# Kernel optimization log

Measured on AMD Instinct MI355X. Metric: run time of the kernel, lower is better.

Reference implementation:

```python
import jax, jax.numpy as jnp
import numpy as np

N, IN_C, HEADS, OUT_C = 100000, 128, 4, 64
E = 1600000
NEG_SLOPE = 0.2
BN_EPS = 1e-5


def setup_inputs() -> dict:
    key = jax.random.key(0)
    ks = jax.random.split(key, 8)
    x = jax.random.normal(ks[0], (N, IN_C), dtype=jnp.float32)
    edge_index = jax.random.randint(ks[1], (2, E), 0, N, dtype=jnp.int64)
    glorot = 1.0 / np.sqrt(IN_C)
    W = jax.random.uniform(ks[2], (IN_C, HEADS * OUT_C), dtype=jnp.float32, minval=-glorot, maxval=glorot)
    att_src = jax.random.normal(ks[3], (HEADS, OUT_C), dtype=jnp.float32) * 0.1
    att_dst = jax.random.normal(ks[4], (HEADS, OUT_C), dtype=jnp.float32) * 0.1
    bias = jnp.zeros((HEADS * OUT_C,), dtype=jnp.float32)
    gamma = jnp.ones((HEADS * OUT_C,), dtype=jnp.float32)
    beta = jnp.zeros((HEADS * OUT_C,), dtype=jnp.float32)
    return {"x": x, "edge_index": edge_index, "W": W, "att_src": att_src,
            "att_dst": att_dst, "bias": bias, "gamma": gamma, "beta": beta}


def reference(x, edge_index, W, att_src, att_dst, bias, gamma, beta):
    n = x.shape[0]
    h_dim, c_dim = att_src.shape
    # add self loops
    loops = jnp.arange(n, dtype=edge_index.dtype)
    src = jnp.concatenate([edge_index[0], loops])  # [Et]
    dst = jnp.concatenate([edge_index[1], loops])  # [Et]
    # linear projection per head
    h = (x @ W).reshape(n, h_dim, c_dim)  # [N,H,C]
    a_src = jnp.einsum('nhc,hc->nh', h, att_src)  # [N,H]
    a_dst = jnp.einsum('nhc,hc->nh', h, att_dst)  # [N,H]
    # edge-wise attention logits + LeakyReLU
    e = jax.nn.leaky_relu(a_src[src] + a_dst[dst], NEG_SLOPE)  # [Et,H]
    # segment softmax over destination neighborhoods
    m = jax.ops.segment_max(e, dst, num_segments=n)  # [N,H]
    e = jnp.exp(e - m[dst])
    denom = jax.ops.segment_sum(e, dst, num_segments=n)  # [N,H]
    alpha = e / (denom[dst] + 1e-16)  # [Et,H]
    # weighted scatter-add aggregation
    out = jax.ops.segment_sum(h[src] * alpha[:, :, None], dst, num_segments=n)  # [N,H,C]
    out = out.reshape(n, h_dim * c_dim) + bias
    # BatchNorm (training-mode batch statistics) + ELU
    mean = out.mean(axis=0)
    var = out.var(axis=0)
    out = gamma * (out - mean) * jax.lax.rsqrt(var + BN_EPS) + beta
    return jax.nn.elu(out)
```

## Files before the change

kernel.cpp:

```cpp
#include <hip/hip_runtime.h>

#define IN_C 128
#define HEADS 4
#define OUT_C 64
#define OUT_F 256
#define NEG_SLOPE 0.2f
#define BN_EPS 1e-5f
#define NBUCK 64
#define BSTRIDE 48

typedef __attribute__((ext_vector_type(8))) short short8;
typedef __attribute__((ext_vector_type(4))) float floatx4;

__device__ __forceinline__ unsigned short f2bf(float f) {
    unsigned u = __float_as_uint(f);
    u += 0x7FFF + ((u >> 16) & 1);
    return (unsigned short)(u >> 16);
}
__device__ __forceinline__ float bf2f(unsigned short u) {
    return __uint_as_float(((unsigned)u) << 16);
}

__global__ void wtprep_kernel(const float* __restrict__ W, unsigned short* __restrict__ Wp)
{
    int idx = blockIdx.x * blockDim.x + threadIdx.x;
    int j  = idx & 7;
    int l  = (idx >> 3) & 63;
    int nt = (idx >> 9) & 3;
    int kt = (idx >> 11) & 3;
    int w  = idx >> 13;
    int k   = kt * 32 + (l >> 4) * 8 + j;
    int col = w * 64 + nt * 16 + (l & 15);
    Wp[idx] = f2bf(W[(size_t)k * OUT_F + col]);
}

__global__ __launch_bounds__(256) void gemm_build_kernel(
    const float* __restrict__ x, const unsigned short* __restrict__ Wp,
    const float* __restrict__ att_src, const float* __restrict__ att_dst,
    unsigned short* __restrict__ h, float* __restrict__ a_src, float* __restrict__ a_dst,
    const int* __restrict__ ei, int* __restrict__ deg, int* __restrict__ srcs,
    int nbg, int n, int E)
{
    if ((int)blockIdx.x >= nbg) {
        int e = ((int)blockIdx.x - nbg) * 256 + (int)threadIdx.x;
        if (e < E) {
            int s = ei[e];
            int d = ei[E + e];
            int pos = atomicAdd(&deg[d], 1);
            if (pos < BSTRIDE) srcs[d * BSTRIDE + pos] = s;
        }
        return;
    }

    __shared__ unsigned short As[16][144];
    __shared__ unsigned short Hs[16][268];

    const int t = threadIdx.x;
    const int w = t >> 6;
    const int l = t & 63;
    const int quad = l >> 4;
    const int c15 = l & 15;
    const int base = blockIdx.x * 16;

    {
        const float4* xs = (const float4*)(x + (size_t)base * IN_C);
#pragma unroll
        for (int i = 0; i < 2; ++i) {
            int idx = t + i * 256;
            float4 v = xs[idx];
            int fi = idx * 4;
            int row = fi >> 7, k = fi & 127;
            ushort4 b;
            b.x = f2bf(v.x); b.y = f2bf(v.y); b.z = f2bf(v.z); b.w = f2bf(v.w);
            *(ushort4*)&As[row][k] = b;
        }
    }

    short8 bfrag[4][4];
#pragma unroll
    for (int kt = 0; kt < 4; ++kt)
#pragma unroll
        for (int nt = 0; nt < 4; ++nt)
            bfrag[kt][nt] = *(const short8*)(Wp + (((w * 4 + kt) * 4 + nt) << 9) + l * 8);

    __syncthreads();

    floatx4 acc[4] = {};
#pragma unroll
    for (int kt = 0; kt < 4; ++kt) {
        int k0 = kt * 32 + quad * 8;
        short8 afrag = *(const short8*)&As[c15][k0];
#pragma unroll
        for (int nt = 0; nt < 4; ++nt)
            acc[nt] = __builtin_amdgcn_mfma_f32_16x16x32_bf16(afrag, bfrag[kt][nt], acc[nt], 0, 0, 0);
    }

    float asum[4] = {0.f, 0.f, 0.f, 0.f}, adsum[4] = {0.f, 0.f, 0.f, 0.f};
#pragma unroll
    for (int nt = 0; nt < 4; ++nt) {
        int col = w * 64 + nt * 16 + c15;
        float aw = att_src[col];
        float dw = att_dst[col];
#pragma unroll
        for (int r = 0; r < 4; ++r) {
            float v = acc[nt][r];
            Hs[quad * 4 + r][col] = f2bf(v);
            asum[r] = fmaf(v, aw, asum[r]);
            adsum[r] = fmaf(v, dw, adsum[r]);
        }
    }
#pragma unroll
    for (int r = 0; r < 4; ++r) {
        float vs = asum[r], vd = adsum[r];
#pragma unroll
        for (int m = 1; m < 16; m <<= 1) {
            vs += __shfl_xor(vs, m, 64);
            vd += __shfl_xor(vd, m, 64);
        }
        if (c15 == 0) {
            int node = base + quad * 4 + r;
            a_src[(size_t)node * HEADS + w] = vs;
            a_dst[(size_t)node * HEADS + w] = vd;
        }
    }

    __syncthreads();
#pragma unroll
    for (int i = 0; i < 2; ++i) {
        int chunk = t + i * 256;
        int si = chunk * 8;
        int row = si >> 8, c0 = si & 255;
        int4 v = *(const int4*)&Hs[row][c0];
        *(int4*)(h + (size_t)(base + row) * OUT_F + c0) = v;
    }
}

__global__ __launch_bounds__(256) void agg_kernel(
    const unsigned short* __restrict__ h, const float* __restrict__ a_src,
    const float* __restrict__ a_dst, const int* __restrict__ deg,
    const int* __restrict__ srcs, const float* __restrict__ bias,
    float* __restrict__ out, float* __restrict__ sbuck, int n)
{
    __shared__ float red[2][4][OUT_F];

    int wave_in_blk = threadIdx.x >> 6;
    int lane = threadIdx.x & 63;
    int dst = blockIdx.x * 4 + wave_in_blk;
    int myh = lane >> 4;
    bool valid = (dst < n);

    float4 o4 = {0.f, 0.f, 0.f, 0.f};

    if (valid) {
        float adh = a_dst[(size_t)dst * HEADS + myh];

        float es = a_src[(size_t)dst * HEADS + myh] + adh;
        es = (es > 0.f) ? es : NEG_SLOPE * es;
        float wgt = __expf(es);
        ushort4 hv = ((const ushort4*)(h + (size_t)dst * OUT_F))[lane];
        float4 acc;
        acc.x = bf2f(hv.x) * wgt; acc.y = bf2f(hv.y) * wgt;
        acc.z = bf2f(hv.z) * wgt; acc.w = bf2f(hv.w) * wgt;
        float wsum = wgt;

        const int start = dst * BSTRIDE;
        int cnt = deg[dst];
        cnt = (cnt > BSTRIDE) ? BSTRIDE : cnt;
        const int last = start + cnt - 1;
        for (int j = 0; j < cnt; j += 8) {
            int rem = cnt - j;
            int s[8];
#pragma unroll
            for (int u = 0; u < 8; ++u) {
                int idx = start + j + u;
                s[u] = srcs[(idx < last) ? idx : last];
            }
            float ew[8];
#pragma unroll
            for (int u = 0; u < 8; ++u) ew[u] = a_src[(size_t)s[u] * HEADS + myh];
            ushort4 hh[8];
#pragma unroll
            for (int u = 0; u < 8; ++u) hh[u] = ((const ushort4*)(h + (size_t)s[u] * OUT_F))[lane];
#pragma unroll
            for (int u = 0; u < 8; ++u) {
                float e = ew[u] + adh;
                e = (e > 0.f) ? e : NEG_SLOPE * e;
                float wv = __expf(e);
                wv = (u < rem) ? wv : 0.f;
                acc.x = fmaf(bf2f(hh[u].x), wv, acc.x);
                acc.y = fmaf(bf2f(hh[u].y), wv, acc.y);
                acc.z = fmaf(bf2f(hh[u].z), wv, acc.z);
                acc.w = fmaf(bf2f(hh[u].w), wv, acc.w);
                wsum += wv;
            }
        }

        float inv = 1.f / (wsum + 1e-16f);
        float4 b4 = ((const float4*)bias)[lane];
        o4.x = fmaf(acc.x, inv, b4.x);
        o4.y = fmaf(acc.y, inv, b4.y);
        o4.z = fmaf(acc.z, inv, b4.z);
        o4.w = fmaf(acc.w, inv, b4.w);
        ((float4*)(out + (size_t)dst * OUT_F))[lane] = o4;
    }

    int c0 = lane * 4;
    *(float4*)&red[0][wave_in_blk][c0] = o4;
    float4 q4;
    q4.x = o4.x * o4.x; q4.y = o4.y * o4.y; q4.z = o4.z * o4.z; q4.w = o4.w * o4.w;
    *(float4*)&red[1][wave_in_blk][c0] = q4;
    __syncthreads();

    int t = threadIdx.x;
    float s  = red[0][0][t] + red[0][1][t] + red[0][2][t] + red[0][3][t];
    float s2 = red[1][0][t] + red[1][1][t] + red[1][2][t] + red[1][3][t];
    float* bk = sbuck + (size_t)(blockIdx.x & (NBUCK - 1)) * (2 * OUT_F);
    atomicAdd(&bk[t], s);
    atomicAdd(&bk[OUT_F + t], s2);
}

__global__ void statsfinal_kernel(const float* __restrict__ sbuck,
                                  const float* __restrict__ gamma,
                                  const float* __restrict__ beta,
                                  float* __restrict__ ss, int n)
{
    int c = threadIdx.x;
    float s = 0.f, s2 = 0.f;
    for (int b = 0; b < NBUCK; ++b) {
        s  += sbuck[(size_t)b * (2 * OUT_F) + c];
        s2 += sbuck[(size_t)b * (2 * OUT_F) + OUT_F + c];
    }
    float invn = 1.f / (float)n;
    float mean = s * invn;
    float var = s2 * invn - mean * mean;
    float sc = gamma[c] * rsqrtf(var + BN_EPS);
    ss[c] = sc;
    ss[OUT_F + c] = beta[c] - mean * sc;
}

__device__ __forceinline__ float elu1(float v) {
    return (v > 0.f) ? v : expm1f(v);
}

__global__ __launch_bounds__(256) void bn_elu_kernel(float* __restrict__ out,
                                                     const float* __restrict__ ss,
                                                     long long n4)
{
    long long idx = (long long)blockIdx.x * blockDim.x + threadIdx.x;
    if (idx >= n4) return;
    int col4 = (int)(idx & 63);
    float4 v = ((float4*)out)[idx];
    float4 sc = ((const float4*)ss)[col4];
    float4 sh = ((const float4*)(ss + OUT_F))[col4];
    v.x = elu1(fmaf(v.x, sc.x, sh.x));
    v.y = elu1(fmaf(v.y, sc.y, sh.y));
    v.z = elu1(fmaf(v.z, sc.z, sh.z));
    v.w = elu1(fmaf(v.w, sc.w, sh.w));
    ((float4*)out)[idx] = v;
}

extern "C" void kernel_launch(void* const* d_in, const int* in_sizes, int n_in,
                              void* d_out, int out_size, void* d_ws, size_t ws_size,
                              hipStream_t stream)
{
    const float* x       = (const float*)d_in[0];
    const int*   ei      = (const int*)d_in[1];
    const float* W       = (const float*)d_in[2];
    const float* att_src = (const float*)d_in[3];
    const float* att_dst = (const float*)d_in[4];
    const float* bias    = (const float*)d_in[5];
    const float* gamma   = (const float*)d_in[6];
    const float* beta    = (const float*)d_in[7];
    float* out = (float*)d_out;

    const int n = in_sizes[0] / IN_C;
    const int E = in_sizes[1] / 2;

    float* ws = (float*)d_ws;
    size_t o = 0;
    unsigned short* h  = (unsigned short*)(ws + o); o += (size_t)n * OUT_F / 2;
    unsigned short* Wp = (unsigned short*)(ws + o); o += IN_C * OUT_F / 2;
    float* a_src  = ws + o; o += (size_t)n * HEADS;
    float* a_dst  = ws + o; o += (size_t)n * HEADS;
    float* ss     = ws + o; o += 2 * OUT_F;
    int* srcs     = (int*)(ws + o); o += (size_t)n * BSTRIDE;
    int* deg      = (int*)(ws + o); o += n;
    float* sbuck  = ws + o; o += (size_t)NBUCK * 2 * OUT_F;

    hipMemsetAsync(deg, 0, ((size_t)n + (size_t)NBUCK * 2 * OUT_F) * sizeof(int), stream);

    const int nbg = (n + 15) / 16;
    const int nbe = (E + 255) / 256;

    wtprep_kernel<<<(IN_C * OUT_F) / 256, 256, 0, stream>>>(W, Wp);
    gemm_build_kernel<<<nbg + nbe, 256, 0, stream>>>(x, Wp, att_src, att_dst,
                                                     h, a_src, a_dst,
                                                     ei, deg, srcs, nbg, n, E);
    agg_kernel<<<(n + 3) / 4, 256, 0, stream>>>(h, a_src, a_dst, deg, srcs, bias, out, sbuck, n);
    statsfinal_kernel<<<1, 256, 0, stream>>>(sbuck, gamma, beta, ss, n);
    bn_elu_kernel<<<(int)(((long long)n * 64 + 255) / 256), 256, 0, stream>>>(out, ss, (long long)n * 64);
}
```

Baseline: 477.5 us.

## Process 64 rows per GEMM block and 8 edges per bucket thread

After: 457.8 us. 1.04x faster.

```diff
diff --git a/kernel.cpp b/kernel.cpp
--- a/kernel.cpp
+++ b/kernel.cpp
@@ -42,12 +42,19 @@
     int nbg, int n, int E)
 {
     if ((int)blockIdx.x >= nbg) {
-        int e = ((int)blockIdx.x - nbg) * 256 + (int)threadIdx.x;
-        if (e < E) {
-            int s = ei[e];
-            int d = ei[E + e];
-            int pos = atomicAdd(&deg[d], 1);
-            if (pos < BSTRIDE) srcs[d * BSTRIDE + pos] = s;
+        int t8 = (((int)blockIdx.x - nbg) * 256 + (int)threadIdx.x) * 8;
+        if (t8 < E) {
+            int4 s0 = *(const int4*)(ei + t8);
+            int4 s1 = *(const int4*)(ei + t8 + 4);
+            int4 d0 = *(const int4*)(ei + E + t8);
+            int4 d1 = *(const int4*)(ei + E + t8 + 4);
+            int ss[8] = {s0.x, s0.y, s0.z, s0.w, s1.x, s1.y, s1.z, s1.w};
+            int dd[8] = {d0.x, d0.y, d0.z, d0.w, d1.x, d1.y, d1.z, d1.w};
+#pragma unroll
+            for (int u = 0; u < 8; ++u) {
+                int pos = atomicAdd(&deg[dd[u]], 1);
+                if (pos < BSTRIDE) srcs[dd[u] * BSTRIDE + pos] = ss[u];
+            }
         }
         return;
     }
@@ -60,78 +67,90 @@
     const int l = t & 63;
     const int quad = l >> 4;
     const int c15 = l & 15;
-    const int base = blockIdx.x * 16;
-
+    const int base = blockIdx.x * 64;
+
+    float4 xv[8];
     {
-        const float4* xs = (const float4*)(x + (size_t)base * IN_C);
+        const size_t maxf4 = (size_t)n * 32 - 1;
+#pragma unroll
+        for (int i = 0; i < 8; ++i) {
+            size_t f4 = (size_t)base * 32 + (size_t)(t + i * 256);
+            xv[i] = ((const float4*)x)[(f4 <= maxf4) ? f4 : maxf4];
+        }
+    }
+
+    short8 bfrag[4][4];
+#pragma unroll
+    for (int kt = 0; kt < 4; ++kt)
+#pragma unroll
+        for (int nt = 0; nt < 4; ++nt)
+            bfrag[kt][nt] = *(const short8*)(Wp + (((w * 4 + kt) * 4 + nt) << 9) + l * 8);
+
+#pragma unroll
+    for (int s = 0; s < 4; ++s) {
+        const int tbase = base + s * 16;
+        if (tbase >= n) break;
+
 #pragma unroll
         for (int i = 0; i < 2; ++i) {
             int idx = t + i * 256;
-            float4 v = xs[idx];
+            float4 v = xv[s * 2 + i];
             int fi = idx * 4;
             int row = fi >> 7, k = fi & 127;
             ushort4 b;
             b.x = f2bf(v.x); b.y = f2bf(v.y); b.z = f2bf(v.z); b.w = f2bf(v.w);
             *(ushort4*)&As[row][k] = b;
         }
-    }
-
-    short8 bfrag[4][4];
-#pragma unroll
-    for (int kt = 0; kt < 4; ++kt)
-#pragma unroll
-        for (int nt = 0; nt < 4; ++nt)
-            bfrag[kt][nt] = *(const short8*)(Wp + (((w * 4 + kt) * 4 + nt) << 9) + l * 8);
-
-    __syncthreads();
-
-    floatx4 acc[4] = {};
-#pragma unroll
-    for (int kt = 0; kt < 4; ++kt) {
-        int k0 = kt * 32 + quad * 8;
-        short8 afrag = *(const short8*)&As[c15][k0];
-#pragma unroll
-        for (int nt = 0; nt < 4; ++nt)
-            acc[nt] = __builtin_amdgcn_mfma_f32_16x16x32_bf16(afrag, bfrag[kt][nt], acc[nt], 0, 0, 0);
-    }
-
-    float asum[4] = {0.f, 0.f, 0.f, 0.f}, adsum[4] = {0.f, 0.f, 0.f, 0.f};
-#pragma unroll
-    for (int nt = 0; nt < 4; ++nt) {
-        int col = w * 64 + nt * 16 + c15;
-        float aw = att_src[col];
-        float dw = att_dst[col];
+        __syncthreads();
+
+        floatx4 acc[4] = {};
+#pragma unroll
+        for (int kt = 0; kt < 4; ++kt) {
+            int k0 = kt * 32 + quad * 8;
+            short8 afrag = *(const short8*)&As[c15][k0];
+#pragma unroll
+            for (int nt = 0; nt < 4; ++nt)
+                acc[nt] = __builtin_amdgcn_mfma_f32_16x16x32_bf16(afrag, bfrag[kt][nt], acc[nt], 0, 0, 0);
+        }
+
+        float asum[4] = {0.f, 0.f, 0.f, 0.f}, adsum[4] = {0.f, 0.f, 0.f, 0.f};
+#pragma unroll
+        for (int nt = 0; nt < 4; ++nt) {
+            int col = w * 64 + nt * 16 + c15;
+            float aw = att_src[col];
+            float dw = att_dst[col];
+#pragma unroll
+            for (int r = 0; r < 4; ++r) {
+                float v = acc[nt][r];
+                Hs[quad * 4 + r][col] = f2bf(v);
+                asum[r] = fmaf(v, aw, asum[r]);
+                adsum[r] = fmaf(v, dw, adsum[r]);
+            }
+        }
 #pragma unroll
         for (int r = 0; r < 4; ++r) {
-            float v = acc[nt][r];
-            Hs[quad * 4 + r][col] = f2bf(v);
-            asum[r] = fmaf(v, aw, asum[r]);
-            adsum[r] = fmaf(v, dw, adsum[r]);
-        }
-    }
-#pragma unroll
-    for (int r = 0; r < 4; ++r) {
-        float vs = asum[r], vd = adsum[r];
-#pragma unroll
-        for (int m = 1; m < 16; m <<= 1) {
-            vs += __shfl_xor(vs, m, 64);
-            vd += __shfl_xor(vd, m, 64);
-        }
-        if (c15 == 0) {
-            int node = base + quad * 4 + r;
-            a_src[(size_t)node * HEADS + w] = vs;
-            a_dst[(size_t)node * HEADS + w] = vd;
-        }
-    }
-
-    __syncthreads();
-#pragma unroll
-    for (int i = 0; i < 2; ++i) {
-        int chunk = t + i * 256;
-        int si = chunk * 8;
-        int row = si >> 8, c0 = si & 255;
-        int4 v = *(const int4*)&Hs[row][c0];
-        *(int4*)(h + (size_t)(base + row) * OUT_F + c0) = v;
+            float vs = asum[r], vd = adsum[r];
+#pragma unroll
+            for (int m = 1; m < 16; m <<= 1) {
+                vs += __shfl_xor(vs, m, 64);
+                vd += __shfl_xor(vd, m, 64);
+            }
+            if (c15 == 0) {
+                int node = tbase + quad * 4 + r;
+                a_src[(size_t)node * HEADS + w] = vs;
+                a_dst[(size_t)node * HEADS + w] = vd;
+            }
+        }
+        __syncthreads();
+
+#pragma unroll
+        for (int i = 0; i < 2; ++i) {
+            int chunk = t + i * 256;
+            int si = chunk * 8;
+            int row = si >> 8, c0 = si & 255;
+            int4 v = *(const int4*)&Hs[row][c0];
+            *(int4*)(h + (size_t)(tbase + row) * OUT_F + c0) = v;
+        }
     }
 }
 
@@ -289,8 +308,8 @@
 
     hipMemsetAsync(deg, 0, ((size_t)n + (size_t)NBUCK * 2 * OUT_F) * sizeof(int), stream);
 
-    const int nbg = (n + 15) / 16;
-    const int nbe = (E + 255) / 256;
+    const int nbg = (n + 63) / 64;
+    const int nbe = (E + 2047) / 2048;
 
     wtprep_kernel<<<(IN_C * OUT_F) / 256, 256, 0, stream>>>(W, Wp);
     gemm_build_kernel<<<nbg + nbe, 256, 0, stream>>>(x, Wp, att_src, att_dst,
```
